# Performance work log

Hardware: AMD Instinct MI355X
Metric: run time of the kernel (lower is better)

The kernel has to match this reference:

```python
import jax, jax.numpy as jnp
import numpy as np

H = 8  # num_heads
EPS = 1e-5


def _lin_params(key, din, dout, scale=0.02):
    kw, _ = jax.random.split(key)
    W = jax.random.normal(kw, (din, dout), jnp.float32) * scale
    b = jnp.zeros((dout,), jnp.float32)
    return W, b


def _edge_attention(x_src, x_dst, ei, ea, Wq, bq, Wk, bk, Wv, bv, We, be, Wo, bo, n_dst):
    out_c = Wq.shape[1]
    D = out_c // H
    scale = D ** -0.5
    q = (x_dst @ Wq + bq).reshape(-1, H, D)
    k = (x_src @ Wk + bk).reshape(-1, H, D)
    v = (x_src @ Wv + bv).reshape(-1, H, D)
    e = (ea @ We + be).reshape(-1, H, D)
    src, dst = ei[0], ei[1]
    ke = k[src] + e                                # [E,H,D]
    ve = v[src] + e                                # [E,H,D]
    s = jnp.einsum('ehd,ehd->eh', q[dst], ke) * scale  # [E,H]
    # segment (per-destination) softmax, numerically stable
    m = jax.ops.segment_max(s, dst, num_segments=n_dst)
    ex = jnp.exp(s - m[dst])
    den = jax.ops.segment_sum(ex, dst, num_segments=n_dst)
    a = ex / den[dst]                              # [E,H]  (dropout = identity in eval)
    agg = jax.ops.segment_sum(a[..., None] * ve, dst, num_segments=n_dst)  # [N_dst,H,D]
    return agg.reshape(n_dst, out_c) @ Wo + bo


def _layernorm(x, g, b):
    mu = jnp.mean(x, axis=-1, keepdims=True)
    var = jnp.mean((x - mu) ** 2, axis=-1, keepdims=True)
    return (x - mu) * jax.lax.rsqrt(var + EPS) * g + b


def setup_inputs() -> dict:
    key = jax.random.key(0)
    ks = jax.random.split(key, 32)
    N_pc, N_gr, E_pp, E_pg = 50000, 8000, 400000, 100000
    din, dout, de = 128, 128, 64
    inp = {}
    inp['x_pc'] = jax.random.normal(ks[0], (N_pc, din), jnp.float32)
    inp['x_gr'] = jax.random.normal(ks[1], (N_gr, din), jnp.float32)
    inp['ea_pp'] = jax.random.normal(ks[2], (E_pp, de), jnp.float32)
    inp['ea_pg'] = jax.random.normal(ks[3], (E_pg, de), jnp.float32)
    inp['ei_pp'] = jax.random.randint(ks[4], (2, E_pp), 0, N_pc, jnp.int32)
    src_pg = jax.random.randint(ks[5], (E_pg,), 0, N_pc, jnp.int32)
    dst_pg = jax.random.randint(ks[6], (E_pg,), 0, N_gr, jnp.int32)
    inp['ei_pg'] = jnp.stack([src_pg, dst_pg])
    i = 7
    for et in ('pp', 'pg'):
        for nm, d_in in (('Wq', din), ('Wk', din), ('Wv', din), ('We', de), ('Wo', dout)):
            W, b = _lin_params(ks[i], d_in, dout); i += 1
            inp[f'{nm}_{et}'] = W
            inp[f'b{nm[1].lower()}_{et}'] = b
    for nt, d_in in (('pc', din), ('gr', din)):
        W, b = _lin_params(ks[i], d_in, dout); i += 1
        inp[f'Wnp_{nt}'] = W
        inp[f'bnp_{nt}'] = b
        inp[f'g_{nt}'] = jnp.ones((dout,), jnp.float32)
        inp[f'bln_{nt}'] = jnp.zeros((dout,), jnp.float32)
    return inp


def reference(x_pc, x_gr, ea_pp, ea_pg, ei_pp, ei_pg,
              Wq_pp, bq_pp, Wk_pp, bk_pp, Wv_pp, bv_pp, We_pp, be_pp, Wo_pp, bo_pp,
              Wq_pg, bq_pg, Wk_pg, bk_pg, Wv_pg, bv_pg, We_pg, be_pg, Wo_pg, bo_pg,
              Wnp_pc, bnp_pc, Wnp_gr, bnp_gr, g_pc, bln_pc, g_gr, bln_gr):
    N_pc, N_gr = x_pc.shape[0], x_gr.shape[0]
    out_pc = x_pc @ Wnp_pc + bnp_pc
    out_gr = x_gr @ Wnp_gr + bnp_gr
    out_pc = out_pc + _edge_attention(x_pc, x_pc, ei_pp, ea_pp,
                                      Wq_pp, bq_pp, Wk_pp, bk_pp, Wv_pp, bv_pp,
                                      We_pp, be_pp, Wo_pp, bo_pp, N_pc)
    out_gr = out_gr + _edge_attention(x_pc, x_gr, ei_pg, ea_pg,
                                      Wq_pg, bq_pg, Wk_pg, bk_pg, Wv_pg, bv_pg,
                                      We_pg, be_pg, Wo_pg, bo_pg, N_gr)
    out_pc = _layernorm(out_pc, g_pc, bln_pc)
    out_gr = _layernorm(out_gr, g_gr, bln_gr)
    return out_pc, out_gr
```

## Files before the change

### kernel.cpp

```cpp
#include <hip/hip_runtime.h>
#include <hip/hip_bf16.h>
#include <stdint.h>

typedef short short8 __attribute__((ext_vector_type(8)));
typedef float f32x4 __attribute__((ext_vector_type(4)));

__device__ __forceinline__ unsigned short f2bf(float x) {
    unsigned u = __float_as_uint(x);
    u += 0x7fffu + ((u >> 16) & 1u);
    return (unsigned short)(u >> 16);
}
__device__ __forceinline__ float bflo(unsigned u) { return __uint_as_float(u << 16); }
__device__ __forceinline__ float bfhi(unsigned u) { return __uint_as_float(u & 0xffff0000u); }

struct WDesc { const float* src; unsigned short* dst; int K, ldd, koff, perm; };
struct WPack { WDesc w[12]; };

__global__ __launch_bounds__(256) void prep_and_count(WPack p,
        const int* __restrict__ d0, int E0, int* c0,
        const int* __restrict__ d1, int E1, int* c1, int nPrep) {
    if ((int)blockIdx.x < nPrep) {
        int wi = blockIdx.x >> 2, chunk = blockIdx.x & 3;
        WDesc d = p.w[wi];
        int total = d.K * 128, cs = total >> 2;
        int lo = chunk * cs, hi = lo + cs;
        for (int i = lo + threadIdx.x; i < hi; i += 256) {
            int n = i / d.K, k = i - n * d.K;
            int kk = d.perm ? (2 * (k & 63) + (k >> 6)) : k;
            d.dst[(size_t)n * d.ldd + d.koff + kk] = f2bf(d.src[(size_t)k * 128 + n]);
        }
    } else {
        int t = (blockIdx.x - nPrep) * 256 + threadIdx.x;
        if (t < E0) atomicAdd(&c0[d0[t]], 1);
        else if (t < E0 + E1) atomicAdd(&c1[d1[t - E0]], 1);
    }
}

struct NodeOut { const unsigned short* Wt; const float* bias; unsigned int* out; int ldc, coloff; };
struct NodePack { NodeOut d[5]; int nout; };

__global__ __launch_bounds__(256) void gemm_node(const float* __restrict__ A0, int M0, NodePack p0,
                                                 int B0,
                                                 const float* __restrict__ A1, int M1, NodePack p1) {
    constexpr int K = 128, LDA = 136, LDB = 72, TLD = 133;
    __shared__ __align__(16) unsigned short As[64 * LDA];
    __shared__ __align__(16) unsigned short Bs[128 * LDB];

    const float* A; int M; NodePack dp; int blk;
    if ((int)blockIdx.x < B0) { A = A0; M = M0; dp = p0; blk = blockIdx.x; }
    else { A = A1; M = M1; dp = p1; blk = blockIdx.x - B0; }

    const int tid = threadIdx.x;
    const int rbase = blk * 64;

    for (int slot = tid; slot < 64 * 16; slot += 256) {
        int row = slot >> 4, kg = slot & 15;
        int gr = rbase + row;
        short8 s8 = {0, 0, 0, 0, 0, 0, 0, 0};
        if (gr < M) {
            const float* a = A + (size_t)gr * K + kg * 8;
            float4 f0 = *reinterpret_cast<const float4*>(a);
            float4 f1 = *reinterpret_cast<const float4*>(a + 4);
            s8[0] = (short)f2bf(f0.x); s8[1] = (short)f2bf(f0.y);
            s8[2] = (short)f2bf(f0.z); s8[3] = (short)f2bf(f0.w);
            s8[4] = (short)f2bf(f1.x); s8[5] = (short)f2bf(f1.y);
            s8[6] = (short)f2bf(f1.z); s8[7] = (short)f2bf(f1.w);
        }
        *reinterpret_cast<short8*>(&As[row * LDA + kg * 8]) = s8;
    }

    const int lane = tid & 63, w = tid >> 6;
    const int rb = (w >> 1) * 32, cb = (w & 1) * 64;
    const int qd = lane >> 4, l16 = lane & 15;

    for (int o = 0; o < dp.nout; ++o) {
        NodeOut d = dp.d[o];
        f32x4 acc[2][4];
#pragma unroll
        for (int rt = 0; rt < 2; ++rt)
#pragma unroll
            for (int ct = 0; ct < 4; ++ct) { f32x4 z = {0.f,0.f,0.f,0.f}; acc[rt][ct] = z; }

        for (int kc = 0; kc < K; kc += 64) {
            __syncthreads();
            for (int slot = tid; slot < 128 * 8; slot += 256) {
                int n = slot >> 3, kg = slot & 7;
                *reinterpret_cast<short8*>(&Bs[n * LDB + kg * 8]) =
                    *reinterpret_cast<const short8*>(d.Wt + (size_t)n * K + kc + kg * 8);
            }
            __syncthreads();
#pragma unroll
            for (int ks = 0; ks < 64; ks += 32) {
                short8 af[2], bfr[4];
#pragma unroll
                for (int rt = 0; rt < 2; ++rt)
                    af[rt] = *reinterpret_cast<const short8*>(
                        &As[(rb + rt * 16 + l16) * LDA + kc + ks + qd * 8]);
#pragma unroll
                for (int ct = 0; ct < 4; ++ct)
                    bfr[ct] = *reinterpret_cast<const short8*>(
                        &Bs[(cb + ct * 16 + l16) * LDB + ks + qd * 8]);
#pragma unroll
                for (int rt = 0; rt < 2; ++rt)
#pragma unroll
                    for (int ct = 0; ct < 4; ++ct)
                        acc[rt][ct] = __builtin_amdgcn_mfma_f32_16x16x32_bf16(
                            af[rt], bfr[ct], acc[rt][ct], 0, 0, 0);
            }
        }

        __syncthreads();
        unsigned short* tile = Bs;
#pragma unroll
        for (int ct = 0; ct < 4; ++ct) {
            int col = cb + ct * 16 + l16;
            float bv = d.bias[col];
#pragma unroll
            for (int rt = 0; rt < 2; ++rt)
#pragma unroll
                for (int r = 0; r < 4; ++r)
                    tile[(rb + rt * 16 + qd * 4 + r) * TLD + col] = f2bf(acc[rt][ct][r] + bv);
        }
        __syncthreads();
#pragma unroll
        for (int rep = 0; rep < 4; ++rep) {
            int lrow = (tid >> 4) + rep * 16, seg = tid & 15;
            int gr = rbase + lrow;
            if (gr < M) {
                uint4 pk;
#pragma unroll
                for (int j = 0; j < 4; ++j) {
                    int pcol = seg * 4 + j;
                    unsigned lo16 = tile[lrow * TLD + pcol];
                    unsigned hi16 = tile[lrow * TLD + pcol + 64];
                    ((unsigned*)&pk)[j] = lo16 | (hi16 << 16);
                }
                *reinterpret_cast<uint4*>(&d.out[(size_t)gr * d.ldc + d.coloff + seg * 4]) = pk;
            }
        }
    }
}

struct EdgePack {
    const float* A; const unsigned short* Wt; const float* bias;
    const int* pos; unsigned int* out; int M;
};

__global__ __launch_bounds__(256) void gemm_edge(EdgePack p0, EdgePack p1, int B0) {
    constexpr int K = 64, LDA = 72, LDB = 72, TLD = 133;
    __shared__ __align__(16) unsigned short As[64 * LDA];
    __shared__ __align__(16) unsigned short Bs[128 * LDB];

    EdgePack p; int blk;
    if ((int)blockIdx.x < B0) { p = p0; blk = blockIdx.x; } else { p = p1; blk = blockIdx.x - B0; }

    const int tid = threadIdx.x;
    const int rbase = blk * 64;

    for (int slot = tid; slot < 64 * 8; slot += 256) {
        int row = slot >> 3, kg = slot & 7;
        int gr = rbase + row;
        short8 s8 = {0, 0, 0, 0, 0, 0, 0, 0};
        if (gr < p.M) {
            const float* a = p.A + (size_t)gr * K + kg * 8;
            float4 f0 = *reinterpret_cast<const float4*>(a);
            float4 f1 = *reinterpret_cast<const float4*>(a + 4);
            s8[0] = (short)f2bf(f0.x); s8[1] = (short)f2bf(f0.y);
            s8[2] = (short)f2bf(f0.z); s8[3] = (short)f2bf(f0.w);
            s8[4] = (short)f2bf(f1.x); s8[5] = (short)f2bf(f1.y);
            s8[6] = (short)f2bf(f1.z); s8[7] = (short)f2bf(f1.w);
        }
        *reinterpret_cast<short8*>(&As[row * LDA + kg * 8]) = s8;
    }
    for (int slot = tid; slot < 128 * 8; slot += 256) {
        int n = slot >> 3, kg = slot & 7;
        *reinterpret_cast<short8*>(&Bs[n * LDB + kg * 8]) =
            *reinterpret_cast<const short8*>(p.Wt + (size_t)n * K + kg * 8);
    }
    __syncthreads();

    const int lane = tid & 63, w = tid >> 6;
    const int rb = (w >> 1) * 32, cb = (w & 1) * 64;
    const int qd = lane >> 4, l16 = lane & 15;

    f32x4 acc[2][4];
#pragma unroll
    for (int rt = 0; rt < 2; ++rt)
#pragma unroll
        for (int ct = 0; ct < 4; ++ct) { f32x4 z = {0.f,0.f,0.f,0.f}; acc[rt][ct] = z; }

#pragma unroll
    for (int ks = 0; ks < 64; ks += 32) {
        short8 af[2], bfr[4];
#pragma unroll
        for (int rt = 0; rt < 2; ++rt)
            af[rt] = *reinterpret_cast<const short8*>(&As[(rb + rt * 16 + l16) * LDA + ks + qd * 8]);
#pragma unroll
        for (int ct = 0; ct < 4; ++ct)
            bfr[ct] = *reinterpret_cast<const short8*>(&Bs[(cb + ct * 16 + l16) * LDB + ks + qd * 8]);
#pragma unroll
        for (int rt = 0; rt < 2; ++rt)
#pragma unroll
            for (int ct = 0; ct < 4; ++ct)
                acc[rt][ct] = __builtin_amdgcn_mfma_f32_16x16x32_bf16(
                    af[rt], bfr[ct], acc[rt][ct], 0, 0, 0);
    }

    __syncthreads();
    unsigned short* tile = Bs;
#pragma unroll
    for (int ct = 0; ct < 4; ++ct) {
        int col = cb + ct * 16 + l16;
        float bv = p.bias[col];
#pragma unroll
        for (int rt = 0; rt < 2; ++rt)
#pragma unroll
            for (int r = 0; r < 4; ++r)
                tile[(rb + rt * 16 + qd * 4 + r) * TLD + col] = f2bf(acc[rt][ct][r] + bv);
    }
    __syncthreads();
#pragma unroll
    for (int rep = 0; rep < 4; ++rep) {
        int lrow = (tid >> 4) + rep * 16, seg = tid & 15;
        int gr = rbase + lrow;
        if (gr < p.M) {
            int dpos = p.pos[gr];
            uint4 pk;
#pragma unroll
            for (int j = 0; j < 4; ++j) {
                int pcol = seg * 4 + j;
                unsigned lo16 = tile[lrow * TLD + pcol];
                unsigned hi16 = tile[lrow * TLD + pcol + 64];
                ((unsigned*)&pk)[j] = lo16 | (hi16 << 16);
            }
            *reinterpret_cast<uint4*>(&p.out[(size_t)dpos * 64 + seg * 4]) = pk;
        }
    }
}

struct OutPack {
    const unsigned short* Aagg; const float* Ax;
    const unsigned short* Wt;
    const float *bo, *bnp, *g, *bln; float* out; int M;
};

__global__ __launch_bounds__(256) void gemm_out_ln(OutPack p0, OutPack p1, int B0) {
    constexpr int K = 256, LDA = 264, LDB = 72, FTLD = 132;
    __shared__ __align__(16) char smemA[64 * LDA * 2];
    __shared__ __align__(16) unsigned short Bs[128 * LDB];
    unsigned short* As = (unsigned short*)smemA;

    OutPack p; int blk;
    if ((int)blockIdx.x < B0) { p = p0; blk = blockIdx.x; } else { p = p1; blk = blockIdx.x - B0; }

    const int tid = threadIdx.x;
    const int rbase = blk * 64;

    for (int slot = tid; slot < 64 * 32; slot += 256) {
        int row = slot >> 5, kg = slot & 31;
        int gr = rbase + row;
        short8 s8 = {0, 0, 0, 0, 0, 0, 0, 0};
        if (gr < p.M) {
            if (kg < 16) {
                s8 = *reinterpret_cast<const short8*>(p.Aagg + (size_t)gr * 128 + kg * 8);
            } else {
                const float* a = p.Ax + (size_t)gr * 128 + (kg - 16) * 8;
                float4 f0 = *reinterpret_cast<const float4*>(a);
                float4 f1 = *reinterpret_cast<const float4*>(a + 4);
                s8[0] = (short)f2bf(f0.x); s8[1] = (short)f2bf(f0.y);
                s8[2] = (short)f2bf(f0.z); s8[3] = (short)f2bf(f0.w);
                s8[4] = (short)f2bf(f1.x); s8[5] = (short)f2bf(f1.y);
                s8[6] = (short)f2bf(f1.z); s8[7] = (short)f2bf(f1.w);
            }
        }
        *reinterpret_cast<short8*>(&As[row * LDA + kg * 8]) = s8;
    }

    const int lane = tid & 63, w = tid >> 6;
    const int rb = (w >> 1) * 32, cb = (w & 1) * 64;
    const int qd = lane >> 4, l16 = lane & 15;

    f32x4 acc[2][4];
#pragma unroll
    for (int rt = 0; rt < 2; ++rt)
#pragma unroll
        for (int ct = 0; ct < 4; ++ct) { f32x4 z = {0.f,0.f,0.f,0.f}; acc[rt][ct] = z; }

    for (int kc = 0; kc < K; kc += 64) {
        __syncthreads();
        for (int slot = tid; slot < 128 * 8; slot += 256) {
            int n = slot >> 3, kg = slot & 7;
            *reinterpret_cast<short8*>(&Bs[n * LDB + kg * 8]) =
                *reinterpret_cast<const short8*>(p.Wt + (size_t)n * K + kc + kg * 8);
        }
        __syncthreads();
#pragma unroll
        for (int ks = 0; ks < 64; ks += 32) {
            short8 af[2], bfr[4];
#pragma unroll
            for (int rt = 0; rt < 2; ++rt)
                af[rt] = *reinterpret_cast<const short8*>(
                    &As[(rb + rt * 16 + l16) * LDA + kc + ks + qd * 8]);
#pragma unroll
            for (int ct = 0; ct < 4; ++ct)
                bfr[ct] = *reinterpret_cast<const short8*>(
                    &Bs[(cb + ct * 16 + l16) * LDB + ks + qd * 8]);
#pragma unroll
            for (int rt = 0; rt < 2; ++rt)
#pragma unroll
                for (int ct = 0; ct < 4; ++ct)
                    acc[rt][ct] = __builtin_amdgcn_mfma_f32_16x16x32_bf16(
                        af[rt], bfr[ct], acc[rt][ct], 0, 0, 0);
        }
    }

    __syncthreads();
    float* ftile = (float*)smemA;
#pragma unroll
    for (int ct = 0; ct < 4; ++ct) {
        int col = cb + ct * 16 + l16;
        float bv = p.bo[col] + p.bnp[col];
#pragma unroll
        for (int rt = 0; rt < 2; ++rt)
#pragma unroll
            for (int r = 0; r < 4; ++r)
                ftile[(rb + rt * 16 + qd * 4 + r) * FTLD + col] = acc[rt][ct][r] + bv;
    }
    __syncthreads();

    int r = tid >> 2, q4 = tid & 3;
    const float* rowp = &ftile[r * FTLD + q4 * 32];
    float s = 0.f, sq = 0.f;
#pragma unroll
    for (int j = 0; j < 8; ++j) {
        float4 v = *reinterpret_cast<const float4*>(rowp + j * 4);
        s += v.x + v.y + v.z + v.w;
        sq += v.x * v.x + v.y * v.y + v.z * v.z + v.w * v.w;
    }
    s += __shfl_xor(s, 1, 64);  s += __shfl_xor(s, 2, 64);
    sq += __shfl_xor(sq, 1, 64); sq += __shfl_xor(sq, 2, 64);
    float mu = s * (1.f / 128.f);
    float var = sq * (1.f / 128.f) - mu * mu;
    float rs = rsqrtf(var + 1e-5f);
    int gr = rbase + r;
    if (gr < p.M) {
#pragma unroll
        for (int j = 0; j < 8; ++j) {
            float4 v = *reinterpret_cast<const float4*>(rowp + j * 4);
            int c = q4 * 32 + j * 4;
            float4 gg = *reinterpret_cast<const float4*>(p.g + c);
            float4 bb = *reinterpret_cast<const float4*>(p.bln + c);
            float4 o;
            o.x = (v.x - mu) * rs * gg.x + bb.x;
            o.y = (v.y - mu) * rs * gg.y + bb.y;
            o.z = (v.z - mu) * rs * gg.z + bb.z;
            o.w = (v.w - mu) * rs * gg.w + bb.w;
            *reinterpret_cast<float4*>(&p.out[(size_t)gr * 128 + c]) = o;
        }
    }
}

__global__ __launch_bounds__(1024) void scan_partial(const int* c0, int N0, int* rp0, int* bs0, int B0,
                                                     const int* c1, int N1, int* rp1, int* bs1) {
    __shared__ int wsum[16];
    const int* c; int* rp; int* bs; int N; int blk;
    if ((int)blockIdx.x < B0) { c = c0; rp = rp0; bs = bs0; N = N0; blk = blockIdx.x; }
    else { c = c1; rp = rp1; bs = bs1; N = N1; blk = blockIdx.x - B0; }
    int tid = threadIdx.x, lane = tid & 63, w = tid >> 6;
    int i = blk * 1024 + tid;
    int v = (i < N) ? c[i] : 0;
    int s = v;
#pragma unroll
    for (int off = 1; off < 64; off <<= 1) {
        int t = __shfl_up(s, off, 64);
        if (lane >= off) s += t;
    }
    if (lane == 63) wsum[w] = s;
    __syncthreads();
    if (w == 0 && lane < 16) {
        int ws = wsum[lane];
#pragma unroll
        for (int off = 1; off < 16; off <<= 1) {
            int t = __shfl_up(ws, off, 64);
            if (lane >= off) ws += t;
        }
        wsum[lane] = ws;
    }
    __syncthreads();
    int wexcl = (w == 0) ? 0 : wsum[w - 1];
    if (i < N) rp[i] = wexcl + s - v;
    if (tid == 0) bs[blk] = wsum[15];
}

__global__ __launch_bounds__(128) void scan_mid(const int* bs0, int* off0, int B0, int* rpN0,
                                                const int* bs1, int* off1, int B1, int* rpN1) {
    int w = threadIdx.x >> 6, lane = threadIdx.x & 63;
    const int* bs = w ? bs1 : bs0;
    int* off = w ? off1 : off0;
    int B = w ? B1 : B0;
    int* rpN = w ? rpN1 : rpN0;
    int v = (lane < B) ? bs[lane] : 0;
    int s = v;
#pragma unroll
    for (int o = 1; o < 64; o <<= 1) {
        int t = __shfl_up(s, o, 64);
        if (lane >= o) s += t;
    }
    if (lane < B) off[lane] = s - v;
    int total = __shfl(s, B - 1, 64);
    if (lane == 0) *rpN = total;
}

__global__ __launch_bounds__(1024) void scan_add(int* rp0, int* cur0, const int* off0, int N0, int B0,
                                                 int* rp1, int* cur1, const int* off1, int N1) {
    int* rp; int* cur; const int* off; int N; int blk;
    if ((int)blockIdx.x < B0) { rp = rp0; cur = cur0; off = off0; N = N0; blk = blockIdx.x; }
    else { rp = rp1; cur = cur1; off = off1; N = N1; blk = blockIdx.x - B0; }
    int i = blk * 1024 + threadIdx.x;
    if (i < N) {
        int vv = rp[i] + off[blk];
        rp[i] = vv;
        cur[i] = vv;
    }
}

__global__ __launch_bounds__(256) void scatter_both(
    const int* __restrict__ s0, const int* __restrict__ d0, int E0, int* cur0, int* pos0, int* srcs0,
    const int* __restrict__ s1, const int* __restrict__ d1, int E1, int* cur1, int* pos1, int* srcs1) {
    int t = blockIdx.x * 256 + threadIdx.x;
    if (t < E0) {
        int p = atomicAdd(&cur0[d0[t]], 1);
        pos0[t] = p;
        srcs0[p] = s0[t];
    } else if (t < E0 + E1) {
        int tt = t - E0;
        int p = atomicAdd(&cur1[d1[tt]], 1);
        pos1[tt] = p;
        srcs1[p] = s1[tt];
    }
}

struct AttnPack {
    const unsigned int *q, *kv, *e;
    const int *srcs;
    const int *row_ptr;
    unsigned int* agg; int N;
};

__global__ __launch_bounds__(256) void attn_gather(AttnPack a0, AttnPack a1, int B0) {
    AttnPack a; int blk;
    if ((int)blockIdx.x < B0) { a = a0; blk = blockIdx.x; } else { a = a1; blk = blockIdx.x - B0; }
    int dst = blk * 4 + (threadIdx.x >> 6);
    if (dst >= a.N) return;
    int lane = threadIdx.x & 63;

    unsigned qp = a.q[(size_t)dst * 64 + lane];
    float qlo = bflo(qp), qhi = bfhi(qp);
    int beg = a.row_ptr[dst], end = a.row_ptr[dst + 1];
    float denl = 0.f, denh = 0.f, accl = 0.f, acch = 0.f;

    int s0 = a.srcs[beg], s1 = a.srcs[beg + 1];
    unsigned k0 = a.kv[(size_t)s0 * 128 + lane];
    unsigned v0 = a.kv[(size_t)s0 * 128 + 64 + lane];
    unsigned e0 = a.e[(size_t)beg * 64 + lane];
    unsigned k1 = a.kv[(size_t)s1 * 128 + lane];
    unsigned v1 = a.kv[(size_t)s1 * 128 + 64 + lane];
    unsigned e1 = a.e[(size_t)(beg + 1) * 64 + lane];

    for (int i = beg; i < end; i += 2) {
        int sn0 = a.srcs[i + 2], sn1 = a.srcs[i + 3];
        unsigned kn0 = a.kv[(size_t)sn0 * 128 + lane];
        unsigned vn0 = a.kv[(size_t)sn0 * 128 + 64 + lane];
        unsigned en0 = a.e[(size_t)(i + 2) * 64 + lane];
        unsigned kn1 = a.kv[(size_t)sn1 * 128 + lane];
        unsigned vn1 = a.kv[(size_t)sn1 * 128 + 64 + lane];
        unsigned en1 = a.e[(size_t)(i + 3) * 64 + lane];

        float e0l = bflo(e0), e0h = bfhi(e0);
        float e1l = bflo(e1), e1h = bfhi(e1);
        float p0l = qlo * (bflo(k0) + e0l), p0h = qhi * (bfhi(k0) + e0h);
        float p1l = qlo * (bflo(k1) + e1l), p1h = qhi * (bfhi(k1) + e1h);
#pragma unroll
        for (int m = 1; m < 16; m <<= 1) {
            p0l += __shfl_xor(p0l, m, 64);
            p0h += __shfl_xor(p0h, m, 64);
            p1l += __shfl_xor(p1l, m, 64);
            p1h += __shfl_xor(p1h, m, 64);
        }
        float x0l = __expf(p0l * 0.25f), x0h = __expf(p0h * 0.25f);
        float x1l = __expf(p1l * 0.25f), x1h = __expf(p1h * 0.25f);
        bool second = (i + 1 < end);
        x1l = second ? x1l : 0.f;
        x1h = second ? x1h : 0.f;
        denl += x0l + x1l;
        denh += x0h + x1h;
        accl += x0l * (bflo(v0) + e0l) + x1l * (bflo(v1) + e1l);
        acch += x0h * (bfhi(v0) + e0h) + x1h * (bfhi(v1) + e1h);
        k0 = kn0; v0 = vn0; e0 = en0;
        k1 = kn1; v1 = vn1; e1 = en1;
    }
    float ol = denl > 0.f ? accl / denl : 0.f;
    float oh = denh > 0.f ? acch / denh : 0.f;
    a.agg[(size_t)dst * 64 + lane] = (unsigned)f2bf(ol) | ((unsigned)f2bf(oh) << 16);
}

extern "C" void kernel_launch(void* const* d_in, const int* in_sizes, int n_in,
                              void* d_out, int out_size, void* d_ws, size_t ws_size,
                              hipStream_t stream) {
    const float* x_pc  = (const float*)d_in[0];
    const float* x_gr  = (const float*)d_in[1];
    const float* ea_pp = (const float*)d_in[2];
    const float* ea_pg = (const float*)d_in[3];
    const int* ei_pp   = (const int*)d_in[4];
    const int* ei_pg   = (const int*)d_in[5];
    const float *Wq_pp = (const float*)d_in[6],  *bq_pp = (const float*)d_in[7];
    const float *Wk_pp = (const float*)d_in[8],  *bk_pp = (const float*)d_in[9];
    const float *Wv_pp = (const float*)d_in[10], *bv_pp = (const float*)d_in[11];
    const float *We_pp = (const float*)d_in[12], *be_pp = (const float*)d_in[13];
    const float *Wo_pp = (const float*)d_in[14], *bo_pp = (const float*)d_in[15];
    const float *Wq_pg = (const float*)d_in[16], *bq_pg = (const float*)d_in[17];
    const float *Wk_pg = (const float*)d_in[18], *bk_pg = (const float*)d_in[19];
    const float *Wv_pg = (const float*)d_in[20], *bv_pg = (const float*)d_in[21];
    const float *We_pg = (const float*)d_in[22], *be_pg = (const float*)d_in[23];
    const float *Wo_pg = (const float*)d_in[24], *bo_pg = (const float*)d_in[25];
    const float *Wnp_pc = (const float*)d_in[26], *bnp_pc = (const float*)d_in[27];
    const float *g_pc   = (const float*)d_in[28], *bln_pc = (const float*)d_in[29];
    const float *Wnp_gr = (const float*)d_in[30], *bnp_gr = (const float*)d_in[31];
    const float *g_gr   = (const float*)d_in[32], *bln_gr = (const float*)d_in[33];

    const int N_pc = in_sizes[0] / 128;
    const int N_gr = in_sizes[1] / 128;
    const int E_pp = in_sizes[4] / 2;
    const int E_pg = in_sizes[5] / 2;

    char* ws = (char*)d_ws;
    size_t off = 0;
    auto alloc = [&](size_t bytes) -> char* {
        char* p = ws + off;
        off += (bytes + 255) & ~(size_t)255;
        return p;
    };
    unsigned short* Wt_q_pp = (unsigned short*)alloc(128 * 128 * 2);
    unsigned short* Wt_k_pp = (unsigned short*)alloc(128 * 128 * 2);
    unsigned short* Wt_v_pp = (unsigned short*)alloc(128 * 128 * 2);
    unsigned short* Wt_k_pg = (unsigned short*)alloc(128 * 128 * 2);
    unsigned short* Wt_v_pg = (unsigned short*)alloc(128 * 128 * 2);
    unsigned short* Wt_q_pg = (unsigned short*)alloc(128 * 128 * 2);
    unsigned short* Wt_e_pp = (unsigned short*)alloc(64 * 128 * 2);
    unsigned short* Wt_e_pg = (unsigned short*)alloc(64 * 128 * 2);
    unsigned short* Wt_cat_pp = (unsigned short*)alloc(256 * 128 * 2);
    unsigned short* Wt_cat_gr = (unsigned short*)alloc(256 * 128 * 2);

    unsigned int* q_pp  = (unsigned int*)alloc((size_t)N_pc * 64 * 4);
    unsigned int* kv_pp = (unsigned int*)alloc((size_t)N_pc * 128 * 4);
    unsigned int* q_pg  = (unsigned int*)alloc((size_t)N_gr * 64 * 4);
    unsigned int* kv_pg = (unsigned int*)alloc((size_t)N_pc * 128 * 4);
    unsigned int* e_pp  = (unsigned int*)alloc((size_t)(E_pp + 4) * 64 * 4);
    unsigned int* e_pg  = (unsigned int*)alloc((size_t)(E_pg + 4) * 64 * 4);
    unsigned int* agg_pp = (unsigned int*)alloc((size_t)N_pc * 64 * 4);
    unsigned int* agg_pg = (unsigned int*)alloc((size_t)N_gr * 64 * 4);
    int* row_ptr_pp = (int*)alloc((size_t)(N_pc + 1) * 4);
    int* cursor_pp  = (int*)alloc((size_t)N_pc * 4);
    int* pos_pp     = (int*)alloc((size_t)E_pp * 4);
    int* row_ptr_pg = (int*)alloc((size_t)(N_gr + 1) * 4);
    int* cursor_pg  = (int*)alloc((size_t)N_gr * 4);
    int* pos_pg     = (int*)alloc((size_t)E_pg * 4);
    int* bsum_pp    = (int*)alloc(64 * 4);
    int* boff_pp    = (int*)alloc(64 * 4);
    int* bsum_pg    = (int*)alloc(64 * 4);
    int* boff_pg    = (int*)alloc(64 * 4);
    char* zbase = ws + off;
    int* counts_pp = (int*)alloc((size_t)N_pc * 4);
    int* counts_pg = (int*)alloc((size_t)N_gr * 4);
    int* srcs_pp   = (int*)alloc((size_t)(E_pp + 8) * 4);
    int* srcs_pg   = (int*)alloc((size_t)(E_pg + 8) * 4);
    size_t zbytes = (size_t)((ws + off) - zbase);
    hipMemsetAsync(zbase, 0, zbytes, stream);
    hipMemsetAsync(e_pp + (size_t)E_pp * 64, 0, 4 * 64 * 4, stream);
    hipMemsetAsync(e_pg + (size_t)E_pg * 64, 0, 4 * 64 * 4, stream);

    float* out_pc = (float*)d_out;
    float* out_gr = out_pc + (size_t)N_pc * 128;

    const int* src_pp = ei_pp;
    const int* dst_pp = ei_pp + E_pp;
    const int* src_pg = ei_pg;
    const int* dst_pg = ei_pg + E_pg;

    WPack wp;
    wp.w[0]  = {Wq_pp, Wt_q_pp, 128, 128, 0, 0};
    wp.w[1]  = {Wk_pp, Wt_k_pp, 128, 128, 0, 0};
    wp.w[2]  = {Wv_pp, Wt_v_pp, 128, 128, 0, 0};
    wp.w[3]  = {Wk_pg, Wt_k_pg, 128, 128, 0, 0};
    wp.w[4]  = {Wv_pg, Wt_v_pg, 128, 128, 0, 0};
    wp.w[5]  = {Wq_pg, Wt_q_pg, 128, 128, 0, 0};
    wp.w[6]  = {We_pp, Wt_e_pp, 64, 64, 0, 0};
    wp.w[7]  = {We_pg, Wt_e_pg, 64, 64, 0, 0};
    wp.w[8]  = {Wo_pp, Wt_cat_pp, 128, 256, 0, 1};
    wp.w[9]  = {Wnp_pc, Wt_cat_pp, 128, 256, 128, 0};
    wp.w[10] = {Wo_pg, Wt_cat_gr, 128, 256, 0, 1};
    wp.w[11] = {Wnp_gr, Wt_cat_gr, 128, 256, 128, 0};
    const int NPREP = 48;
    const int gE = (E_pp + E_pg + 255) / 256;
    prep_and_count<<<NPREP + gE, 256, 0, stream>>>(wp, dst_pp, E_pp, counts_pp,
                                                   dst_pg, E_pg, counts_pg, NPREP);

    const int Bs_pp = (N_pc + 1023) / 1024, Bs_pg = (N_gr + 1023) / 1024;
    scan_partial<<<Bs_pp + Bs_pg, 1024, 0, stream>>>(counts_pp, N_pc, row_ptr_pp, bsum_pp, Bs_pp,
                                                     counts_pg, N_gr, row_ptr_pg, bsum_pg);
    scan_mid<<<1, 128, 0, stream>>>(bsum_pp, boff_pp, Bs_pp, &row_ptr_pp[N_pc],
                                    bsum_pg, boff_pg, Bs_pg, &row_ptr_pg[N_gr]);
    scan_add<<<Bs_pp + Bs_pg, 1024, 0, stream>>>(row_ptr_pp, cursor_pp, boff_pp, N_pc, Bs_pp,
                                                 row_ptr_pg, cursor_pg, boff_pg, N_gr);
    scatter_both<<<gE, 256, 0, stream>>>(src_pp, dst_pp, E_pp, cursor_pp, pos_pp, srcs_pp,
                                         src_pg, dst_pg, E_pg, cursor_pg, pos_pg, srcs_pg);

    NodePack np;
    np.d[0] = {Wt_q_pp, bq_pp, q_pp, 64, 0};
    np.d[1] = {Wt_k_pp, bk_pp, kv_pp, 128, 0};
    np.d[2] = {Wt_v_pp, bv_pp, kv_pp, 128, 64};
    np.d[3] = {Wt_k_pg, bk_pg, kv_pg, 128, 0};
    np.d[4] = {Wt_v_pg, bv_pg, kv_pg, 128, 64};
    np.nout = 5;
    NodePack ng{};
    ng.d[0] = {Wt_q_pg, bq_pg, q_pg, 64, 0};
    ng.nout = 1;
    int Bn0 = (N_pc + 63) / 64, Bn1 = (N_gr + 63) / 64;
    gemm_node<<<Bn0 + Bn1, 256, 0, stream>>>(x_pc, N_pc, np, Bn0, x_gr, N_gr, ng);

    EdgePack ep0 = {ea_pp, Wt_e_pp, be_pp, pos_pp, e_pp, E_pp};
    EdgePack ep1 = {ea_pg, Wt_e_pg, be_pg, pos_pg, e_pg, E_pg};
    int Be0 = (E_pp + 63) / 64, Be1 = (E_pg + 63) / 64;
    gemm_edge<<<Be0 + Be1, 256, 0, stream>>>(ep0, ep1, Be0);

    AttnPack ap0 = {q_pp, kv_pp, e_pp, srcs_pp, row_ptr_pp, agg_pp, N_pc};
    AttnPack ap1 = {q_pg, kv_pg, e_pg, srcs_pg, row_ptr_pg, agg_pg, N_gr};
    int Ba0 = (N_pc + 3) / 4, Ba1 = (N_gr + 3) / 4;
    attn_gather<<<Ba0 + Ba1, 256, 0, stream>>>(ap0, ap1, Ba0);

    OutPack op0 = {(const unsigned short*)agg_pp, x_pc, Wt_cat_pp, bo_pp, bnp_pc, g_pc, bln_pc, out_pc, N_pc};
    OutPack op1 = {(const unsigned short*)agg_pg, x_gr, Wt_cat_gr, bo_pg, bnp_gr, g_gr, bln_gr, out_gr, N_gr};
    int Bo0 = (N_pc + 63) / 64, Bo1 = (N_gr + 63) / 64;
    gemm_out_ln<<<Bo0 + Bo1, 256, 0, stream>>>(op0, op1, Bo0);
}
```

Baseline: 521.1 us.

## Make edge GEMM persistent with register-prefetched A tiles and direct epilogue stores

The edge-attribute projection becomes a persistent kernel with a fixed grid of 1024 blocks, split between the two edge types in proportion to their tile counts. Each block loads the weight tile and bias into LDS and registers once, then loops over row tiles, prefetching the next tile's fp32 activations into registers while the MFMAs for the current tile run. The epilogue is also changed: the LDS transpose is dropped and each lane writes packed bf16 pairs straight to the scattered destination rows, with a column permutation of B so lo/hi halves land in the same lane. This cuts per-block weight reloads and launch overhead and hides global load latency, at the cost of narrower 4-byte scattered stores and extra barriers per tile.

```diff
diff --git a/kernel.cpp b/kernel.cpp
--- a/kernel.cpp
+++ b/kernel.cpp
@@ -143,98 +143,147 @@
 
 struct EdgePack {
     const float* A; const unsigned short* Wt; const float* bias;
-    const int* pos; unsigned int* out; int M;
+    const int* pos; unsigned int* out; int M; int nTiles;
 };
 
-__global__ __launch_bounds__(256) void gemm_edge(EdgePack p0, EdgePack p1, int B0) {
-    constexpr int K = 64, LDA = 72, LDB = 72, TLD = 133;
+__global__ __launch_bounds__(256, 5) void gemm_edge(EdgePack p0, EdgePack p1, int G0, int G1) {
+    constexpr int LDA = 72, LDB = 72;
     __shared__ __align__(16) unsigned short As[64 * LDA];
     __shared__ __align__(16) unsigned short Bs[128 * LDB];
 
-    EdgePack p; int blk;
-    if ((int)blockIdx.x < B0) { p = p0; blk = blockIdx.x; } else { p = p1; blk = blockIdx.x - B0; }
+    EdgePack p; int blk, stride;
+    if ((int)blockIdx.x < G0) { p = p0; blk = blockIdx.x; stride = G0; }
+    else { p = p1; blk = blockIdx.x - G0; stride = G1; }
+    if (blk >= p.nTiles) return;
 
     const int tid = threadIdx.x;
-    const int rbase = blk * 64;
-
-    for (int slot = tid; slot < 64 * 8; slot += 256) {
-        int row = slot >> 3, kg = slot & 7;
-        int gr = rbase + row;
-        short8 s8 = {0, 0, 0, 0, 0, 0, 0, 0};
-        if (gr < p.M) {
-            const float* a = p.A + (size_t)gr * K + kg * 8;
-            float4 f0 = *reinterpret_cast<const float4*>(a);
-            float4 f1 = *reinterpret_cast<const float4*>(a + 4);
-            s8[0] = (short)f2bf(f0.x); s8[1] = (short)f2bf(f0.y);
-            s8[2] = (short)f2bf(f0.z); s8[3] = (short)f2bf(f0.w);
-            s8[4] = (short)f2bf(f1.x); s8[5] = (short)f2bf(f1.y);
-            s8[6] = (short)f2bf(f1.z); s8[7] = (short)f2bf(f1.w);
-        }
-        *reinterpret_cast<short8*>(&As[row * LDA + kg * 8]) = s8;
-    }
+    const int lane = tid & 63, w = tid >> 6;
+    const int rb = (w >> 1) * 32;
+    const int qd = lane >> 4, l16 = lane & 15;
+    const int r0 = tid >> 3, r1 = r0 + 32, kg = tid & 7;
+
     for (int slot = tid; slot < 128 * 8; slot += 256) {
-        int n = slot >> 3, kg = slot & 7;
-        *reinterpret_cast<short8*>(&Bs[n * LDB + kg * 8]) =
-            *reinterpret_cast<const short8*>(p.Wt + (size_t)n * K + kg * 8);
+        int n = slot >> 3, k8 = slot & 7;
+        *reinterpret_cast<short8*>(&Bs[n * LDB + k8 * 8]) =
+            *reinterpret_cast<const short8*>(p.Wt + (size_t)n * 64 + k8 * 8);
+    }
+    float bvlo[2], bvhi[2];
+#pragma unroll
+    for (int cq = 0; cq < 2; ++cq) {
+        int pc = (w & 1) * 32 + cq * 16 + l16;
+        bvlo[cq] = p.bias[pc];
+        bvhi[cq] = p.bias[pc + 64];
+    }
+
+    const float4 z4 = {0.f, 0.f, 0.f, 0.f};
+    float4 a00, a01, a10, a11;
+
+    {
+        int tb = blk * 64;
+        a00 = z4; a01 = z4; a10 = z4; a11 = z4;
+        if (tb + r0 < p.M) {
+            const float* a = p.A + (size_t)(tb + r0) * 64 + kg * 8;
+            a00 = *reinterpret_cast<const float4*>(a);
+            a01 = *reinterpret_cast<const float4*>(a + 4);
+        }
+        if (tb + r1 < p.M) {
+            const float* a = p.A + (size_t)(tb + r1) * 64 + kg * 8;
+            a10 = *reinterpret_cast<const float4*>(a);
+            a11 = *reinterpret_cast<const float4*>(a + 4);
+        }
+        short8 s;
+        s[0] = (short)f2bf(a00.x); s[1] = (short)f2bf(a00.y);
+        s[2] = (short)f2bf(a00.z); s[3] = (short)f2bf(a00.w);
+        s[4] = (short)f2bf(a01.x); s[5] = (short)f2bf(a01.y);
+        s[6] = (short)f2bf(a01.z); s[7] = (short)f2bf(a01.w);
+        *reinterpret_cast<short8*>(&As[r0 * LDA + kg * 8]) = s;
+        s[0] = (short)f2bf(a10.x); s[1] = (short)f2bf(a10.y);
+        s[2] = (short)f2bf(a10.z); s[3] = (short)f2bf(a10.w);
+        s[4] = (short)f2bf(a11.x); s[5] = (short)f2bf(a11.y);
+        s[6] = (short)f2bf(a11.z); s[7] = (short)f2bf(a11.w);
+        *reinterpret_cast<short8*>(&As[r1 * LDA + kg * 8]) = s;
     }
     __syncthreads();
 
-    const int lane = tid & 63, w = tid >> 6;
-    const int rb = (w >> 1) * 32, cb = (w & 1) * 64;
-    const int qd = lane >> 4, l16 = lane & 15;
-
-    f32x4 acc[2][4];
-#pragma unroll
-    for (int rt = 0; rt < 2; ++rt)
-#pragma unroll
-        for (int ct = 0; ct < 4; ++ct) { f32x4 z = {0.f,0.f,0.f,0.f}; acc[rt][ct] = z; }
-
-#pragma unroll
-    for (int ks = 0; ks < 64; ks += 32) {
-        short8 af[2], bfr[4];
+    for (int t = blk; t < p.nTiles; t += stride) {
+        int tn = t + stride;
+        int tl = (tn < p.nTiles) ? tn : t;
+        {
+            int tb = tl * 64;
+            a00 = z4; a01 = z4; a10 = z4; a11 = z4;
+            if (tb + r0 < p.M) {
+                const float* a = p.A + (size_t)(tb + r0) * 64 + kg * 8;
+                a00 = *reinterpret_cast<const float4*>(a);
+                a01 = *reinterpret_cast<const float4*>(a + 4);
+            }
+            if (tb + r1 < p.M) {
+                const float* a = p.A + (size_t)(tb + r1) * 64 + kg * 8;
+                a10 = *reinterpret_cast<const float4*>(a);
+                a11 = *reinterpret_cast<const float4*>(a + 4);
+            }
+        }
+
+        f32x4 acc[2][4];
 #pragma unroll
         for (int rt = 0; rt < 2; ++rt)
-            af[rt] = *reinterpret_cast<const short8*>(&As[(rb + rt * 16 + l16) * LDA + ks + qd * 8]);
-#pragma unroll
-        for (int ct = 0; ct < 4; ++ct)
-            bfr[ct] = *reinterpret_cast<const short8*>(&Bs[(cb + ct * 16 + l16) * LDB + ks + qd * 8]);
-#pragma unroll
-        for (int rt = 0; rt < 2; ++rt)
-#pragma unroll
-            for (int ct = 0; ct < 4; ++ct)
-                acc[rt][ct] = __builtin_amdgcn_mfma_f32_16x16x32_bf16(
-                    af[rt], bfr[ct], acc[rt][ct], 0, 0, 0);
-    }
-
-    __syncthreads();
-    unsigned short* tile = Bs;
-#pragma unroll
-    for (int ct = 0; ct < 4; ++ct) {
-        int col = cb + ct * 16 + l16;
-        float bv = p.bias[col];
-#pragma unroll
-        for (int rt = 0; rt < 2; ++rt)
-#pragma unroll
-            for (int r = 0; r < 4; ++r)
-                tile[(rb + rt * 16 + qd * 4 + r) * TLD + col] = f2bf(acc[rt][ct][r] + bv);
-    }
-    __syncthreads();
-#pragma unroll
-    for (int rep = 0; rep < 4; ++rep) {
-        int lrow = (tid >> 4) + rep * 16, seg = tid & 15;
-        int gr = rbase + lrow;
-        if (gr < p.M) {
-            int dpos = p.pos[gr];
-            uint4 pk;
-#pragma unroll
-            for (int j = 0; j < 4; ++j) {
-                int pcol = seg * 4 + j;
-                unsigned lo16 = tile[lrow * TLD + pcol];
-                unsigned hi16 = tile[lrow * TLD + pcol + 64];
-                ((unsigned*)&pk)[j] = lo16 | (hi16 << 16);
+#pragma unroll
+            for (int ct = 0; ct < 4; ++ct) { f32x4 z = {0.f,0.f,0.f,0.f}; acc[rt][ct] = z; }
+#pragma unroll
+        for (int ks = 0; ks < 64; ks += 32) {
+            short8 af[2], bfr[4];
+#pragma unroll
+            for (int rt = 0; rt < 2; ++rt)
+                af[rt] = *reinterpret_cast<const short8*>(
+                    &As[(rb + rt * 16 + l16) * LDA + ks + qd * 8]);
+#pragma unroll
+            for (int ct = 0; ct < 4; ++ct) {
+                int nb = (w & 1) * 32 + (ct & 1) * 64 + (ct >> 1) * 16;
+                bfr[ct] = *reinterpret_cast<const short8*>(
+                    &Bs[(nb + l16) * LDB + ks + qd * 8]);
             }
-            *reinterpret_cast<uint4*>(&p.out[(size_t)dpos * 64 + seg * 4]) = pk;
-        }
+#pragma unroll
+            for (int rt = 0; rt < 2; ++rt)
+#pragma unroll
+                for (int ct = 0; ct < 4; ++ct)
+                    acc[rt][ct] = __builtin_amdgcn_mfma_f32_16x16x32_bf16(
+                        af[rt], bfr[ct], acc[rt][ct], 0, 0, 0);
+        }
+
+        {
+            int tb = t * 64;
+#pragma unroll
+            for (int rt = 0; rt < 2; ++rt)
+#pragma unroll
+                for (int r = 0; r < 4; ++r) {
+                    int row = rb + rt * 16 + qd * 4 + r;
+                    int gr = tb + row;
+                    if (gr < p.M) {
+                        int dpos = p.pos[gr];
+#pragma unroll
+                        for (int cq = 0; cq < 2; ++cq) {
+                            unsigned lo = f2bf(acc[rt][cq * 2][r] + bvlo[cq]);
+                            unsigned hi = f2bf(acc[rt][cq * 2 + 1][r] + bvhi[cq]);
+                            p.out[(size_t)dpos * 64 + (w & 1) * 32 + cq * 16 + l16] =
+                                lo | (hi << 16);
+                        }
+                    }
+                }
+        }
+        __syncthreads();
+        {
+            short8 s;
+            s[0] = (short)f2bf(a00.x); s[1] = (short)f2bf(a00.y);
+            s[2] = (short)f2bf(a00.z); s[3] = (short)f2bf(a00.w);
+            s[4] = (short)f2bf(a01.x); s[5] = (short)f2bf(a01.y);
+            s[6] = (short)f2bf(a01.z); s[7] = (short)f2bf(a01.w);
+            *reinterpret_cast<short8*>(&As[r0 * LDA + kg * 8]) = s;
+            s[0] = (short)f2bf(a10.x); s[1] = (short)f2bf(a10.y);
+            s[2] = (short)f2bf(a10.z); s[3] = (short)f2bf(a10.w);
+            s[4] = (short)f2bf(a11.x); s[5] = (short)f2bf(a11.y);
+            s[6] = (short)f2bf(a11.z); s[7] = (short)f2bf(a11.w);
+            *reinterpret_cast<short8*>(&As[r1 * LDA + kg * 8]) = s;
+        }
+        __syncthreads();
     }
 }
 
@@ -628,10 +677,17 @@
     int Bn0 = (N_pc + 63) / 64, Bn1 = (N_gr + 63) / 64;
     gemm_node<<<Bn0 + Bn1, 256, 0, stream>>>(x_pc, N_pc, np, Bn0, x_gr, N_gr, ng);
 
-    EdgePack ep0 = {ea_pp, Wt_e_pp, be_pp, pos_pp, e_pp, E_pp};
-    EdgePack ep1 = {ea_pg, Wt_e_pg, be_pg, pos_pg, e_pg, E_pg};
-    int Be0 = (E_pp + 63) / 64, Be1 = (E_pg + 63) / 64;
-    gemm_edge<<<Be0 + Be1, 256, 0, stream>>>(ep0, ep1, Be0);
+    int Te0 = (E_pp + 63) / 64, Te1 = (E_pg + 63) / 64;
+    const int Gtot = 1024;
+    int G0 = (int)((long long)Gtot * Te0 / (Te0 + Te1));
+    if (G0 < 1) G0 = 1;
+    if (G0 > Te0) G0 = Te0;
+    int G1 = Gtot - G0;
+    if (G1 > Te1) G1 = Te1;
+    if (G1 < 1) G1 = 1;
+    EdgePack ep0 = {ea_pp, Wt_e_pp, be_pp, pos_pp, e_pp, E_pp, Te0};
+    EdgePack ep1 = {ea_pg, Wt_e_pg, be_pg, pos_pg, e_pg, E_pg, Te1};
+    gemm_edge<<<G0 + G1, 256, 0, stream>>>(ep0, ep1, G0, G1);
 
     AttnPack ap0 = {q_pp, kv_pp, e_pp, srcs_pp, row_ptr_pp, agg_pp, N_pc};
     AttnPack ap1 = {q_pg, kv_pg, e_pg, srcs_pg, row_ptr_pg, agg_pg, N_gr};
```

New measurement: 529.4 us. Within noise of the previous version (+1.6%).

## Restructure edge GEMM to load A fragments directly into registers and scatter from registers

Applied to the files above, without the earlier changes.

The edge-feature GEMM no longer stages the A tile in shared memory. Each wave now loads its own 32 rows straight from global memory into MFMA fragment registers and computes all 128 output columns. Results are scattered straight from accumulators to permuted positions, which removes the shared-memory transpose tile and two barriers. Blocks now cover 128 rows instead of 64, halving the grid. In exchange the output stores become 4-byte scattered writes instead of 16-byte vector writes, and register pressure rises with 64 accumulator floats per thread.

```diff
diff --git a/kernel.cpp b/kernel.cpp
--- a/kernel.cpp
+++ b/kernel.cpp
@@ -147,95 +147,88 @@
 };
 
 __global__ __launch_bounds__(256) void gemm_edge(EdgePack p0, EdgePack p1, int B0) {
-    constexpr int K = 64, LDA = 72, LDB = 72, TLD = 133;
-    __shared__ __align__(16) unsigned short As[64 * LDA];
+    constexpr int LDB = 72;
     __shared__ __align__(16) unsigned short Bs[128 * LDB];
 
     EdgePack p; int blk;
     if ((int)blockIdx.x < B0) { p = p0; blk = blockIdx.x; } else { p = p1; blk = blockIdx.x - B0; }
 
     const int tid = threadIdx.x;
-    const int rbase = blk * 64;
-
-    for (int slot = tid; slot < 64 * 8; slot += 256) {
-        int row = slot >> 3, kg = slot & 7;
-        int gr = rbase + row;
-        short8 s8 = {0, 0, 0, 0, 0, 0, 0, 0};
-        if (gr < p.M) {
-            const float* a = p.A + (size_t)gr * K + kg * 8;
-            float4 f0 = *reinterpret_cast<const float4*>(a);
-            float4 f1 = *reinterpret_cast<const float4*>(a + 4);
-            s8[0] = (short)f2bf(f0.x); s8[1] = (short)f2bf(f0.y);
-            s8[2] = (short)f2bf(f0.z); s8[3] = (short)f2bf(f0.w);
-            s8[4] = (short)f2bf(f1.x); s8[5] = (short)f2bf(f1.y);
-            s8[6] = (short)f2bf(f1.z); s8[7] = (short)f2bf(f1.w);
-        }
-        *reinterpret_cast<short8*>(&As[row * LDA + kg * 8]) = s8;
-    }
     for (int slot = tid; slot < 128 * 8; slot += 256) {
-        int n = slot >> 3, kg = slot & 7;
-        *reinterpret_cast<short8*>(&Bs[n * LDB + kg * 8]) =
-            *reinterpret_cast<const short8*>(p.Wt + (size_t)n * K + kg * 8);
+        int n = slot >> 3, k8 = slot & 7;
+        *reinterpret_cast<short8*>(&Bs[n * LDB + k8 * 8]) =
+            *reinterpret_cast<const short8*>(p.Wt + (size_t)n * 64 + k8 * 8);
     }
     __syncthreads();
 
     const int lane = tid & 63, w = tid >> 6;
-    const int rb = (w >> 1) * 32, cb = (w & 1) * 64;
     const int qd = lane >> 4, l16 = lane & 15;
-
-    f32x4 acc[2][4];
+    const int rbase = blk * 128 + w * 32;
+    if (rbase >= p.M) return;
+
+    float4 fa[4][2];
 #pragma unroll
     for (int rt = 0; rt < 2; ++rt)
 #pragma unroll
-        for (int ct = 0; ct < 4; ++ct) { f32x4 z = {0.f,0.f,0.f,0.f}; acc[rt][ct] = z; }
-
-#pragma unroll
-    for (int ks = 0; ks < 64; ks += 32) {
-        short8 af[2], bfr[4];
-#pragma unroll
-        for (int rt = 0; rt < 2; ++rt)
-            af[rt] = *reinterpret_cast<const short8*>(&As[(rb + rt * 16 + l16) * LDA + ks + qd * 8]);
-#pragma unroll
-        for (int ct = 0; ct < 4; ++ct)
-            bfr[ct] = *reinterpret_cast<const short8*>(&Bs[(cb + ct * 16 + l16) * LDB + ks + qd * 8]);
-#pragma unroll
-        for (int rt = 0; rt < 2; ++rt)
-#pragma unroll
-            for (int ct = 0; ct < 4; ++ct)
-                acc[rt][ct] = __builtin_amdgcn_mfma_f32_16x16x32_bf16(
-                    af[rt], bfr[ct], acc[rt][ct], 0, 0, 0);
-    }
-
-    __syncthreads();
-    unsigned short* tile = Bs;
+        for (int ks = 0; ks < 2; ++ks) {
+            int gr = rbase + rt * 16 + l16;
+            int grc = gr < p.M ? gr : p.M - 1;
+            const float* a = p.A + (size_t)grc * 64 + ks * 32 + qd * 8;
+            fa[rt * 2 + ks][0] = *reinterpret_cast<const float4*>(a);
+            fa[rt * 2 + ks][1] = *reinterpret_cast<const float4*>(a + 4);
+        }
+
+    short8 af[2][2];
+#pragma unroll
+    for (int rt = 0; rt < 2; ++rt)
+#pragma unroll
+        for (int ks = 0; ks < 2; ++ks) {
+            float4 f0 = fa[rt * 2 + ks][0], f1 = fa[rt * 2 + ks][1];
+            short8 s;
+            s[0] = (short)f2bf(f0.x); s[1] = (short)f2bf(f0.y);
+            s[2] = (short)f2bf(f0.z); s[3] = (short)f2bf(f0.w);
+            s[4] = (short)f2bf(f1.x); s[5] = (short)f2bf(f1.y);
+            s[6] = (short)f2bf(f1.z); s[7] = (short)f2bf(f1.w);
+            af[rt][ks] = s;
+        }
+
+    f32x4 acc[2][8];
+#pragma unroll
+    for (int rt = 0; rt < 2; ++rt)
+#pragma unroll
+        for (int ct = 0; ct < 8; ++ct) { f32x4 z = {0.f,0.f,0.f,0.f}; acc[rt][ct] = z; }
+#pragma unroll
+    for (int ks = 0; ks < 2; ++ks)
+#pragma unroll
+        for (int ct = 0; ct < 8; ++ct) {
+            short8 bf = *reinterpret_cast<const short8*>(
+                &Bs[(ct * 16 + l16) * LDB + ks * 32 + qd * 8]);
+            acc[0][ct] = __builtin_amdgcn_mfma_f32_16x16x32_bf16(af[0][ks], bf, acc[0][ct], 0, 0, 0);
+            acc[1][ct] = __builtin_amdgcn_mfma_f32_16x16x32_bf16(af[1][ks], bf, acc[1][ct], 0, 0, 0);
+        }
+
+    float blo[4], bhi[4];
 #pragma unroll
     for (int ct = 0; ct < 4; ++ct) {
-        int col = cb + ct * 16 + l16;
-        float bv = p.bias[col];
-#pragma unroll
-        for (int rt = 0; rt < 2; ++rt)
-#pragma unroll
-            for (int r = 0; r < 4; ++r)
-                tile[(rb + rt * 16 + qd * 4 + r) * TLD + col] = f2bf(acc[rt][ct][r] + bv);
-    }
-    __syncthreads();
-#pragma unroll
-    for (int rep = 0; rep < 4; ++rep) {
-        int lrow = (tid >> 4) + rep * 16, seg = tid & 15;
-        int gr = rbase + lrow;
-        if (gr < p.M) {
-            int dpos = p.pos[gr];
-            uint4 pk;
-#pragma unroll
-            for (int j = 0; j < 4; ++j) {
-                int pcol = seg * 4 + j;
-                unsigned lo16 = tile[lrow * TLD + pcol];
-                unsigned hi16 = tile[lrow * TLD + pcol + 64];
-                ((unsigned*)&pk)[j] = lo16 | (hi16 << 16);
+        blo[ct] = p.bias[ct * 16 + l16];
+        bhi[ct] = p.bias[64 + ct * 16 + l16];
+    }
+#pragma unroll
+    for (int rt = 0; rt < 2; ++rt)
+#pragma unroll
+        for (int r = 0; r < 4; ++r) {
+            int gr = rbase + rt * 16 + qd * 4 + r;
+            if (gr < p.M) {
+                int dpos = p.pos[gr];
+                unsigned int* dst = p.out + (size_t)dpos * 64 + l16;
+#pragma unroll
+                for (int ct = 0; ct < 4; ++ct) {
+                    unsigned lo = f2bf(acc[rt][ct][r] + blo[ct]);
+                    unsigned hi = f2bf(acc[rt][ct + 4][r] + bhi[ct]);
+                    dst[ct * 16] = lo | (hi << 16);
+                }
             }
-            *reinterpret_cast<uint4*>(&p.out[(size_t)dpos * 64 + seg * 4]) = pk;
-        }
-    }
+        }
 }
 
 struct OutPack {
@@ -630,7 +623,7 @@
 
     EdgePack ep0 = {ea_pp, Wt_e_pp, be_pp, pos_pp, e_pp, E_pp};
     EdgePack ep1 = {ea_pg, Wt_e_pg, be_pg, pos_pg, e_pg, E_pg};
-    int Be0 = (E_pp + 63) / 64, Be1 = (E_pg + 63) / 64;
+    int Be0 = (E_pp + 127) / 128, Be1 = (E_pg + 127) / 128;
     gemm_edge<<<Be0 + Be1, 256, 0, stream>>>(ep0, ep1, Be0);
 
     AttnPack ap0 = {q_pp, kv_pp, e_pp, srcs_pp, row_ptr_pp, agg_pp, N_pc};
```

New measurement: 523.7 us. About the same (+0.5%).
